# Optimization experiments

Measured on AMD Instinct MI355X. Metric: run time of the kernel, lower is better.

Reference implementation:

```python
import jax, jax.numpy as jnp
import numpy as np

B, T, D, H, L = 64, 4096, 128, 128, 2


def setup_inputs() -> dict:
    key = jax.random.key(0)
    ks = jax.random.split(key, 9)
    s = 1.0 / np.sqrt(H)
    return {
        "x": jax.random.normal(ks[0], (B, T, D), dtype=jnp.float32),
        "W_ih0": jax.random.normal(ks[1], (3 * H, D), dtype=jnp.float32) * s,
        "W_hh0": jax.random.normal(ks[2], (3 * H, H), dtype=jnp.float32) * s,
        "b_ih0": jax.random.normal(ks[3], (3 * H,), dtype=jnp.float32) * s,
        "b_hh0": jax.random.normal(ks[4], (3 * H,), dtype=jnp.float32) * s,
        "W_ih1": jax.random.normal(ks[5], (3 * H, H), dtype=jnp.float32) * s,
        "W_hh1": jax.random.normal(ks[6], (3 * H, H), dtype=jnp.float32) * s,
        "b_ih1": jax.random.normal(ks[7], (3 * H,), dtype=jnp.float32) * s,
        "b_hh1": jax.random.normal(ks[8], (3 * H,), dtype=jnp.float32) * s,
    }


def _gru_cell(h, xt, W_ih, W_hh, b_ih, b_hh):
    # torch.nn.GRUCell math; gates packed as [r, z, n] along 3H.
    gi = xt @ W_ih.T + b_ih            # [B, 3H]
    gh = h @ W_hh.T + b_hh             # [B, 3H]
    i_r, i_z, i_n = jnp.split(gi, 3, axis=-1)
    h_r, h_z, h_n = jnp.split(gh, 3, axis=-1)
    r = jax.nn.sigmoid(i_r + h_r)
    z = jax.nn.sigmoid(i_z + h_z)
    n = jnp.tanh(i_n + r * h_n)
    return (1.0 - z) * n + z * h


def reference(x, W_ih0, W_hh0, b_ih0, b_hh0, W_ih1, W_hh1, b_ih1, b_hh1):
    h0 = jnp.zeros((L, x.shape[0], H), dtype=x.dtype)
    params = ((W_ih0, W_hh0, b_ih0, b_hh0), (W_ih1, W_hh1, b_ih1, b_hh1))

    def step(h, xt):
        # h: [L, B, H]; xt: [B, D]
        inp = xt
        new_h = []
        for l in range(L):
            hl = _gru_cell(h[l], inp, *params[l])
            new_h.append(hl)
            inp = hl
        return jnp.stack(new_h, axis=0), None

    xs = jnp.swapaxes(x, 0, 1)  # [T, B, D]
    h_final, _ = jax.lax.scan(step, h0, xs)
    return h_final  # [L, B, H]
```

## Files before the change

### kernel.cpp

```cpp
#include <hip/hip_runtime.h>


#define Tlen 4096
#define Hd   128
#define Bsz  64

typedef __attribute__((ext_vector_type(8))) short short8;
typedef __attribute__((ext_vector_type(4))) short short4v;
typedef __attribute__((ext_vector_type(4))) float float4v;
typedef __attribute__((ext_vector_type(2))) unsigned int uint2v;

#define MFMA16(a, b, c) __builtin_amdgcn_mfma_f32_16x16x32_bf16((a), (b), (c), 0, 0, 0)

static __device__ __forceinline__ float fast_exp2(float x) {
#if __has_builtin(__builtin_amdgcn_exp2f)
  return __builtin_amdgcn_exp2f(x);
#else
  return exp2f(x);
#endif
}
static __device__ __forceinline__ float fast_rcp(float x) {
  return __builtin_amdgcn_rcpf(x);
}
static __device__ __forceinline__ short f2bf(float f) {
  unsigned u = __builtin_bit_cast(unsigned, f);
  u = (u + 0x7FFFu + ((u >> 16) & 1u)) >> 16;
  return (short)u;
}
static __device__ __forceinline__ unsigned pk2bf(float a, float b) {
#if __has_builtin(__builtin_amdgcn_cvt_pk_bf16_f32)
  auto v = __builtin_amdgcn_cvt_pk_bf16_f32(a, b);
  return __builtin_bit_cast(unsigned, v);
#else
  return (unsigned)(unsigned short)f2bf(a) | ((unsigned)(unsigned short)f2bf(b) << 16);
#endif
}
static __device__ __forceinline__ short8 loadw8(const float* __restrict__ p) {
  short8 r;
  #pragma unroll
  for (int j = 0; j < 8; ++j) r[j] = f2bf(p[j]);
  return r;
}

#define XB   0
#define H0B  4096
#define H1B  8192
#define BLK  2048

__global__ __launch_bounds__(512, 2) void gru_scan(
    const float* __restrict__ x,
    const float* __restrict__ Wih0, const float* __restrict__ Whh0,
    const float* __restrict__ bih0, const float* __restrict__ bhh0,
    const float* __restrict__ Wih1, const float* __restrict__ Whh1,
    const float* __restrict__ bih1, const float* __restrict__ bhh1,
    float* __restrict__ out) {
  __shared__ alignas(16) short Abuf[12288];

  const int tid   = threadIdx.x;
  const int wave  = tid >> 6;
  const int lane  = tid & 63;
  const int lc    = lane & 15;
  const int quad  = lane >> 4;
  const int q8    = quad * 8;
  const int lane8 = lane * 8;
  const int bbase = blockIdx.x * 16;

  const int wgrp = wave >> 2;
  const int w4   = wave & 3;

  const float* Wi = wgrp ? Wih1 : Wih0;
  const float* Wh = wgrp ? Whh1 : Whh0;
  const float* bi = wgrp ? bih1 : bih0;
  const float* bh = wgrp ? bhh1 : bhh0;

  short8 fxr[2][4], fxz[2][4], fxn[2][4];
  short8 fhr[2][4], fhz[2][4], fhn[2][4];
  float kr[2], kz[2], ki[2], kh[2];
  const float nL  = -1.44269504088896f;
  const float n2L = -2.88539008177793f;
  #pragma unroll
  for (int G = 0; G < 2; ++G) {
    const int c = 32 * w4 + 16 * G + lc;
    #pragma unroll
    for (int s = 0; s < 4; ++s) {
      const int k = 32 * s + q8;
      fxr[G][s] = loadw8(Wi + (c)       * Hd + k);
      fxz[G][s] = loadw8(Wi + (128 + c) * Hd + k);
      fxn[G][s] = loadw8(Wi + (256 + c) * Hd + k);
      fhr[G][s] = loadw8(Wh + (c)       * Hd + k);
      fhz[G][s] = loadw8(Wh + (128 + c) * Hd + k);
      fhn[G][s] = loadw8(Wh + (256 + c) * Hd + k);
    }
    kr[G] = nL  * (bi[c] + bh[c]);
    kz[G] = nL  * (bi[128 + c] + bh[128 + c]);
    ki[G] = n2L * bi[256 + c];
    kh[G] = n2L * bh[256 + c];
  }

  const int hsel = wgrp ? H1B : H0B;
  const int isel = wgrp ? H0B : XB;

  int hw[2];
  #pragma unroll
  for (int G = 0; G < 2; ++G)
    hw[G] = w4 * 512 + (2 * G + (lc >> 3)) * 128 + (lc & 7);

  const int xrow = tid >> 5;
  const int xk0  = 4 * (tid & 31);
  const int xwoff = (xk0 >> 5) * 512 + ((xk0 >> 3) & 3) * 128 + xrow * 8 + (xk0 & 7);
  const float* xg = x + (size_t)(bbase + xrow) * (Tlen * Hd) + xk0;

  const int glo = wgrp ? 2 : 0;
  const int ghi = glo + Tlen;

  {
    int* zb = (int*)Abuf;
    #pragma unroll
    for (int i = 0; i < 8; ++i) zb[2048 + tid + 512 * i] = 0;
    const float4v v0 = *(const float4v*)(xg);
    const float4v v1 = *(const float4v*)(xg + Hd);
    uint2v p0 = {pk2bf(v0[0], v0[1]), pk2bf(v0[2], v0[3])};
    uint2v p1 = {pk2bf(v1[0], v1[1]), pk2bf(v1[2], v1[3])};
    *(short4v*)&Abuf[XB + xwoff]       = __builtin_bit_cast(short4v, p0);
    *(short4v*)&Abuf[XB + BLK + xwoff] = __builtin_bit_cast(short4v, p1);
  }
  __syncthreads();

  const float4v Z4 = {0.f, 0.f, 0.f, 0.f};
  float4v ar[2], az[2], an[2], ah[2];
  float4v hp[2] = {Z4, Z4};

  #pragma unroll
  for (int G = 0; G < 2; ++G) { ar[G] = Z4; az[G] = Z4; an[G] = Z4; ah[G] = Z4; }
  #pragma unroll
  for (int s = 0; s < 4; ++s) {
    const short8 a = *(const short8*)&Abuf[isel + s * 512 + lane8];
    #pragma unroll
    for (int G = 0; G < 2; ++G) {
      ar[G] = MFMA16(a, fxr[G][s], ar[G]);
      az[G] = MFMA16(a, fxz[G][s], az[G]);
      an[G] = MFMA16(a, fxn[G][s], an[G]);
    }
  }

  for (int t = 0; t < Tlen + 2; ++t) {
    const int par  = (t & 1) * BLK;
    const int parx = BLK - par;

    const int tn = (t + 2 < Tlen) ? (t + 2) : (Tlen - 1);
    const float4v xv = *(const float4v*)(xg + (size_t)tn * Hd);
    const int hrd = hsel + parx;
    #pragma unroll
    for (int s = 0; s < 4; ++s) {
      const short8 a = *(const short8*)&Abuf[hrd + s * 512 + lane8];
      #pragma unroll
      for (int G = 0; G < 2; ++G) {
        ar[G] = MFMA16(a, fhr[G][s], ar[G]);
        az[G] = MFMA16(a, fhz[G][s], az[G]);
        ah[G] = MFMA16(a, fhn[G][s], ah[G]);
      }
    }
    __syncthreads();

    if (t >= glo && t < ghi) {
      const int wr = hsel + par;
      #pragma unroll
      for (int G = 0; G < 2; ++G) {
        #pragma unroll
        for (int i = 0; i < 4; ++i) {
          const float er = fast_exp2(fmaf(ar[G][i], nL, kr[G]));
          const float rr = fast_rcp(1.0f + er);
          const float ez = fast_exp2(fmaf(az[G][i], nL, kz[G]));
          const float zz = fast_rcp(1.0f + ez);
          float vv = fmaf(rr, fmaf(ah[G][i], n2L, kh[G]),
                          fmaf(an[G][i], n2L, ki[G]));
          vv = fminf(vv, 126.0f);
          const float e2 = fast_exp2(vv);
          const float nn = (1.0f - e2) * fast_rcp(1.0f + e2);
          const float hn = fmaf(zz, hp[G][i] - nn, nn);
          hp[G][i] = hn;
          Abuf[wr + hw[G] + (quad * 4 + i) * 8] = f2bf(hn);
        }
      }
    }
    {
      uint2v pp = {pk2bf(xv[0], xv[1]), pk2bf(xv[2], xv[3])};
      *(short4v*)&Abuf[XB + par + xwoff] = __builtin_bit_cast(short4v, pp);
    }
    const int ird = isel + parx;
    #pragma unroll
    for (int G = 0; G < 2; ++G) { ar[G] = Z4; az[G] = Z4; an[G] = Z4; ah[G] = Z4; }
    #pragma unroll
    for (int s = 0; s < 4; ++s) {
      const short8 a = *(const short8*)&Abuf[ird + s * 512 + lane8];
      #pragma unroll
      for (int G = 0; G < 2; ++G) {
        ar[G] = MFMA16(a, fxr[G][s], ar[G]);
        az[G] = MFMA16(a, fxz[G][s], az[G]);
        an[G] = MFMA16(a, fxn[G][s], an[G]);
      }
    }
    __syncthreads();
  }

  #pragma unroll
  for (int G = 0; G < 2; ++G) {
    const int u = 32 * w4 + 16 * G + lc;
    #pragma unroll
    for (int i = 0; i < 4; ++i) {
      const int b = bbase + quad * 4 + i;
      out[wgrp * (Bsz * Hd) + b * Hd + u] = hp[G][i];
    }
  }
}

extern "C" void kernel_launch(void* const* d_in, const int* in_sizes, int n_in,
                              void* d_out, int out_size, void* d_ws, size_t ws_size,
                              hipStream_t stream) {
  (void)in_sizes; (void)n_in; (void)out_size; (void)d_ws; (void)ws_size;
  gru_scan<<<4, 512, 0, stream>>>(
      (const float*)d_in[0],
      (const float*)d_in[1], (const float*)d_in[2],
      (const float*)d_in[3], (const float*)d_in[4],
      (const float*)d_in[5], (const float*)d_in[6],
      (const float*)d_in[7], (const float*)d_in[8],
      (float*)d_out);
}
```

Measured before the change: 7.165 ms.

## Double-buffer gate accumulators and interleave gate math with next-step input MFMAs

Splits the gate accumulators into two ping-pong sets and unrolls the time loop by two, so the next step's input-projection MFMAs can go into fresh registers while the current step's gate nonlinearities are still being computed. The gate math is interleaved between the per-slice input MFMAs so the transcendental/VALU work can overlap with matrix-core work. Accumulator zeroing is folded into the first MFMA. This raises register pressure (an extra set of six float4 accumulators) under a 512-thread, 2-blocks launch bound, which risks spills.

```diff
diff --git a/kernel.cpp b/kernel.cpp
--- a/kernel.cpp
+++ b/kernel.cpp
@@ -46,6 +46,73 @@
 #define H0B  4096
 #define H1B  8192
 #define BLK  2048
+
+#define GATE(CR, CZ, CN, G_, i_, wr_)                                       \
+  {                                                                         \
+    const float er = fast_exp2(fmaf(CR[G_][i_], nL, kr[G_]));               \
+    const float rr = fast_rcp(1.0f + er);                                   \
+    const float ez = fast_exp2(fmaf(CZ[G_][i_], nL, kz[G_]));               \
+    const float zz = fast_rcp(1.0f + ez);                                   \
+    float vv = fmaf(rr, fmaf(ahv[G_][i_], n2L, kh[G_]),                     \
+                    fmaf(CN[G_][i_], n2L, ki[G_]));                         \
+    vv = fminf(vv, 126.0f);                                                 \
+    const float e2 = fast_exp2(vv);                                         \
+    const float nn = (1.0f - e2) * fast_rcp(1.0f + e2);                     \
+    const float hn = fmaf(zz, hp[G_][i_] - nn, nn);                         \
+    hp[G_][i_] = hn;                                                        \
+    Abuf[(wr_) + hw[G_] + (quad * 4 + i_) * 8] = f2bf(hn);                  \
+  }
+
+#define STEP(t_, CR, CZ, CN, NR, NZ, NN)                                    \
+  {                                                                         \
+    const int par  = ((t_) & 1) * BLK;                                      \
+    const int parx = BLK - par;                                             \
+    const int tn = ((t_) + 2 < Tlen) ? ((t_) + 2) : (Tlen - 1);             \
+    const float4v xv = *(const float4v*)(xg + (size_t)tn * Hd);             \
+    const int hrd = hsel + parx;                                            \
+    _Pragma("unroll")                                                       \
+    for (int s = 0; s < 4; ++s) {                                           \
+      const short8 a = *(const short8*)&Abuf[hrd + s * 512 + lane8];        \
+      _Pragma("unroll")                                                     \
+      for (int G = 0; G < 2; ++G) {                                         \
+        CR[G] = MFMA16(a, fhr[G][s], CR[G]);                                \
+        CZ[G] = MFMA16(a, fhz[G][s], CZ[G]);                                \
+        ahv[G] = (s == 0) ? MFMA16(a, fhn[G][0], Z4)                        \
+                          : MFMA16(a, fhn[G][s], ahv[G]);                   \
+      }                                                                     \
+    }                                                                       \
+    __syncthreads();                                                        \
+    {                                                                       \
+      uint2v pp = {pk2bf(xv[0], xv[1]), pk2bf(xv[2], xv[3])};               \
+      *(short4v*)&Abuf[XB + par + xwoff] = __builtin_bit_cast(short4v, pp); \
+    }                                                                       \
+    const bool gv = ((t_) >= glo) & ((t_) < ghi);                           \
+    const int wr  = hsel + par;                                             \
+    const int ird = isel + parx;                                            \
+    _Pragma("unroll")                                                       \
+    for (int s = 0; s < 4; ++s) {                                           \
+      const short8 a = *(const short8*)&Abuf[ird + s * 512 + lane8];        \
+      if (gv) {                                                             \
+        _Pragma("unroll")                                                   \
+        for (int ii = 0; ii < 2; ++ii) {                                    \
+          GATE(CR, CZ, CN, (s >> 1), ((s & 1) * 2 + ii), wr);               \
+        }                                                                   \
+      }                                                                     \
+      _Pragma("unroll")                                                     \
+      for (int G = 0; G < 2; ++G) {                                         \
+        if (s == 0) {                                                       \
+          NR[G] = MFMA16(a, fxr[G][0], Z4);                                 \
+          NZ[G] = MFMA16(a, fxz[G][0], Z4);                                 \
+          NN[G] = MFMA16(a, fxn[G][0], Z4);                                 \
+        } else {                                                            \
+          NR[G] = MFMA16(a, fxr[G][s], NR[G]);                              \
+          NZ[G] = MFMA16(a, fxz[G][s], NZ[G]);                              \
+          NN[G] = MFMA16(a, fxn[G][s], NN[G]);                              \
+        }                                                                   \
+      }                                                                     \
+    }                                                                       \
+    __syncthreads();                                                        \
+  }
 
 __global__ __launch_bounds__(512, 2) void gru_scan(
     const float* __restrict__ x,
@@ -127,80 +194,30 @@
   __syncthreads();
 
   const float4v Z4 = {0.f, 0.f, 0.f, 0.f};
-  float4v ar[2], az[2], an[2], ah[2];
-  float4v hp[2] = {Z4, Z4};
-
-  #pragma unroll
-  for (int G = 0; G < 2; ++G) { ar[G] = Z4; az[G] = Z4; an[G] = Z4; ah[G] = Z4; }
+  float4v arA[2], azA[2], anA[2];
+  float4v arB[2], azB[2], anB[2];
+  float4v ahv[2], hp[2] = {Z4, Z4};
+
   #pragma unroll
   for (int s = 0; s < 4; ++s) {
     const short8 a = *(const short8*)&Abuf[isel + s * 512 + lane8];
     #pragma unroll
     for (int G = 0; G < 2; ++G) {
-      ar[G] = MFMA16(a, fxr[G][s], ar[G]);
-      az[G] = MFMA16(a, fxz[G][s], az[G]);
-      an[G] = MFMA16(a, fxn[G][s], an[G]);
-    }
-  }
-
-  for (int t = 0; t < Tlen + 2; ++t) {
-    const int par  = (t & 1) * BLK;
-    const int parx = BLK - par;
-
-    const int tn = (t + 2 < Tlen) ? (t + 2) : (Tlen - 1);
-    const float4v xv = *(const float4v*)(xg + (size_t)tn * Hd);
-    const int hrd = hsel + parx;
-    #pragma unroll
-    for (int s = 0; s < 4; ++s) {
-      const short8 a = *(const short8*)&Abuf[hrd + s * 512 + lane8];
-      #pragma unroll
-      for (int G = 0; G < 2; ++G) {
-        ar[G] = MFMA16(a, fhr[G][s], ar[G]);
-        az[G] = MFMA16(a, fhz[G][s], az[G]);
-        ah[G] = MFMA16(a, fhn[G][s], ah[G]);
+      if (s == 0) {
+        arA[G] = MFMA16(a, fxr[G][0], Z4);
+        azA[G] = MFMA16(a, fxz[G][0], Z4);
+        anA[G] = MFMA16(a, fxn[G][0], Z4);
+      } else {
+        arA[G] = MFMA16(a, fxr[G][s], arA[G]);
+        azA[G] = MFMA16(a, fxz[G][s], azA[G]);
+        anA[G] = MFMA16(a, fxn[G][s], anA[G]);
       }
     }
-    __syncthreads();
-
-    if (t >= glo && t < ghi) {
-      const int wr = hsel + par;
-      #pragma unroll
-      for (int G = 0; G < 2; ++G) {
-        #pragma unroll
-        for (int i = 0; i < 4; ++i) {
-          const float er = fast_exp2(fmaf(ar[G][i], nL, kr[G]));
-          const float rr = fast_rcp(1.0f + er);
-          const float ez = fast_exp2(fmaf(az[G][i], nL, kz[G]));
-          const float zz = fast_rcp(1.0f + ez);
-          float vv = fmaf(rr, fmaf(ah[G][i], n2L, kh[G]),
-                          fmaf(an[G][i], n2L, ki[G]));
-          vv = fminf(vv, 126.0f);
-          const float e2 = fast_exp2(vv);
-          const float nn = (1.0f - e2) * fast_rcp(1.0f + e2);
-          const float hn = fmaf(zz, hp[G][i] - nn, nn);
-          hp[G][i] = hn;
-          Abuf[wr + hw[G] + (quad * 4 + i) * 8] = f2bf(hn);
-        }
-      }
-    }
-    {
-      uint2v pp = {pk2bf(xv[0], xv[1]), pk2bf(xv[2], xv[3])};
-      *(short4v*)&Abuf[XB + par + xwoff] = __builtin_bit_cast(short4v, pp);
-    }
-    const int ird = isel + parx;
-    #pragma unroll
-    for (int G = 0; G < 2; ++G) { ar[G] = Z4; az[G] = Z4; an[G] = Z4; ah[G] = Z4; }
-    #pragma unroll
-    for (int s = 0; s < 4; ++s) {
-      const short8 a = *(const short8*)&Abuf[ird + s * 512 + lane8];
-      #pragma unroll
-      for (int G = 0; G < 2; ++G) {
-        ar[G] = MFMA16(a, fxr[G][s], ar[G]);
-        az[G] = MFMA16(a, fxz[G][s], az[G]);
-        an[G] = MFMA16(a, fxn[G][s], an[G]);
-      }
-    }
-    __syncthreads();
+  }
+
+  for (int tt = 0; tt < Tlen + 2; tt += 2) {
+    STEP(tt,     arA, azA, anA, arB, azB, anB);
+    STEP(tt + 1, arB, azB, anB, arA, azA, anA);
   }
 
   #pragma unroll
```

After: 13.37 ms. 1.87x slower.

## Stagger layer-0 and layer-1 wave groups across barrier phases to overlap work

Applied to the files above, without the earlier changes.

Reorganizes the per-timestep schedule so the two wave groups (layer 0 and layer 1) do their gate math and MFMAs in opposite halves between the two barriers. Layer 1's elementwise update now runs while layer 0 does its recurrent MFMAs, and the reverse, with layer 1 lagging by an extra step. The aim is to stop both groups from hitting the serial elementwise phase at once, keeping the MFMA and VALU pipes busy together. It also moves x staging to layer-0 waves only, using 8-wide loads and packed bf16 stores. The cost is one extra loop iteration and more complex buffer-parity bookkeeping.

```diff
diff --git a/kernel.cpp b/kernel.cpp
--- a/kernel.cpp
+++ b/kernel.cpp
@@ -8,7 +8,7 @@
 typedef __attribute__((ext_vector_type(8))) short short8;
 typedef __attribute__((ext_vector_type(4))) short short4v;
 typedef __attribute__((ext_vector_type(4))) float float4v;
-typedef __attribute__((ext_vector_type(2))) unsigned int uint2v;
+typedef __attribute__((ext_vector_type(4))) unsigned int uint4v;
 
 #define MFMA16(a, b, c) __builtin_amdgcn_mfma_f32_16x16x32_bf16((a), (b), (c), 0, 0, 0)
 
@@ -34,6 +34,11 @@
 #else
   return (unsigned)(unsigned short)f2bf(a) | ((unsigned)(unsigned short)f2bf(b) << 16);
 #endif
+}
+static __device__ __forceinline__ short8 pk8(float4v a, float4v b) {
+  uint4v u = {pk2bf(a[0], a[1]), pk2bf(a[2], a[3]),
+              pk2bf(b[0], b[1]), pk2bf(b[2], b[3])};
+  return __builtin_bit_cast(short8, u);
 }
 static __device__ __forceinline__ short8 loadw8(const float* __restrict__ p) {
   short8 r;
@@ -105,99 +110,150 @@
   for (int G = 0; G < 2; ++G)
     hw[G] = w4 * 512 + (2 * G + (lc >> 3)) * 128 + (lc & 7);
 
-  const int xrow = tid >> 5;
-  const int xk0  = 4 * (tid & 31);
-  const int xwoff = (xk0 >> 5) * 512 + ((xk0 >> 3) & 3) * 128 + xrow * 8 + (xk0 & 7);
-  const float* xg = x + (size_t)(bbase + xrow) * (Tlen * Hd) + xk0;
-
-  const int glo = wgrp ? 2 : 0;
-  const int ghi = glo + Tlen;
+  const int xrow  = tid >> 4;
+  const int xk0   = (tid & 15) * 8;
+  const int xwoff = (xk0 >> 5) * 512 + ((xk0 >> 3) & 3) * 128 + xrow * 8;
+  const float* xg = x + (size_t)(bbase + (xrow & 15)) * (Tlen * Hd) + xk0;
 
   {
     int* zb = (int*)Abuf;
     #pragma unroll
     for (int i = 0; i < 8; ++i) zb[2048 + tid + 512 * i] = 0;
-    const float4v v0 = *(const float4v*)(xg);
-    const float4v v1 = *(const float4v*)(xg + Hd);
-    uint2v p0 = {pk2bf(v0[0], v0[1]), pk2bf(v0[2], v0[3])};
-    uint2v p1 = {pk2bf(v1[0], v1[1]), pk2bf(v1[2], v1[3])};
-    *(short4v*)&Abuf[XB + xwoff]       = __builtin_bit_cast(short4v, p0);
-    *(short4v*)&Abuf[XB + BLK + xwoff] = __builtin_bit_cast(short4v, p1);
+    if (wgrp == 0) {
+      const float4v a0 = *(const float4v*)(xg);
+      const float4v b0 = *(const float4v*)(xg + 4);
+      const float4v a1 = *(const float4v*)(xg + Hd);
+      const float4v b1 = *(const float4v*)(xg + Hd + 4);
+      *(short8*)&Abuf[XB + xwoff]       = pk8(a0, b0);
+      *(short8*)&Abuf[XB + BLK + xwoff] = pk8(a1, b1);
+    }
   }
   __syncthreads();
 
   const float4v Z4 = {0.f, 0.f, 0.f, 0.f};
   float4v ar[2], az[2], an[2], ah[2];
   float4v hp[2] = {Z4, Z4};
-
   #pragma unroll
   for (int G = 0; G < 2; ++G) { ar[G] = Z4; az[G] = Z4; an[G] = Z4; ah[G] = Z4; }
-  #pragma unroll
-  for (int s = 0; s < 4; ++s) {
-    const short8 a = *(const short8*)&Abuf[isel + s * 512 + lane8];
-    #pragma unroll
-    for (int G = 0; G < 2; ++G) {
-      ar[G] = MFMA16(a, fxr[G][s], ar[G]);
-      az[G] = MFMA16(a, fxz[G][s], az[G]);
-      an[G] = MFMA16(a, fxn[G][s], an[G]);
-    }
-  }
-
-  for (int t = 0; t < Tlen + 2; ++t) {
-    const int par  = (t & 1) * BLK;
-    const int parx = BLK - par;
-
-    const int tn = (t + 2 < Tlen) ? (t + 2) : (Tlen - 1);
-    const float4v xv = *(const float4v*)(xg + (size_t)tn * Hd);
-    const int hrd = hsel + parx;
+
+  if (wgrp == 0) {
     #pragma unroll
     for (int s = 0; s < 4; ++s) {
-      const short8 a = *(const short8*)&Abuf[hrd + s * 512 + lane8];
-      #pragma unroll
-      for (int G = 0; G < 2; ++G) {
-        ar[G] = MFMA16(a, fhr[G][s], ar[G]);
-        az[G] = MFMA16(a, fhz[G][s], az[G]);
-        ah[G] = MFMA16(a, fhn[G][s], ah[G]);
-      }
-    }
-    __syncthreads();
-
-    if (t >= glo && t < ghi) {
-      const int wr = hsel + par;
-      #pragma unroll
-      for (int G = 0; G < 2; ++G) {
-        #pragma unroll
-        for (int i = 0; i < 4; ++i) {
-          const float er = fast_exp2(fmaf(ar[G][i], nL, kr[G]));
-          const float rr = fast_rcp(1.0f + er);
-          const float ez = fast_exp2(fmaf(az[G][i], nL, kz[G]));
-          const float zz = fast_rcp(1.0f + ez);
-          float vv = fmaf(rr, fmaf(ah[G][i], n2L, kh[G]),
-                          fmaf(an[G][i], n2L, ki[G]));
-          vv = fminf(vv, 126.0f);
-          const float e2 = fast_exp2(vv);
-          const float nn = (1.0f - e2) * fast_rcp(1.0f + e2);
-          const float hn = fmaf(zz, hp[G][i] - nn, nn);
-          hp[G][i] = hn;
-          Abuf[wr + hw[G] + (quad * 4 + i) * 8] = f2bf(hn);
-        }
-      }
-    }
-    {
-      uint2v pp = {pk2bf(xv[0], xv[1]), pk2bf(xv[2], xv[3])};
-      *(short4v*)&Abuf[XB + par + xwoff] = __builtin_bit_cast(short4v, pp);
-    }
-    const int ird = isel + parx;
-    #pragma unroll
-    for (int G = 0; G < 2; ++G) { ar[G] = Z4; az[G] = Z4; an[G] = Z4; ah[G] = Z4; }
-    #pragma unroll
-    for (int s = 0; s < 4; ++s) {
-      const short8 a = *(const short8*)&Abuf[ird + s * 512 + lane8];
+      const short8 a = *(const short8*)&Abuf[XB + s * 512 + lane8];
       #pragma unroll
       for (int G = 0; G < 2; ++G) {
         ar[G] = MFMA16(a, fxr[G][s], ar[G]);
         az[G] = MFMA16(a, fxz[G][s], az[G]);
         an[G] = MFMA16(a, fxn[G][s], an[G]);
+      }
+    }
+  }
+
+  for (int t = 0; t < Tlen + 3; ++t) {
+    const int par  = (t & 1) * BLK;
+    const int parx = BLK - par;
+    float4v xv0, xv1;
+
+    if (wgrp == 0) {
+      const int tn = (t + 2 < Tlen) ? (t + 2) : (Tlen - 1);
+      xv0 = *(const float4v*)(xg + (size_t)tn * Hd);
+      xv1 = *(const float4v*)(xg + (size_t)tn * Hd + 4);
+      const int hrd = hsel + parx;
+      #pragma unroll
+      for (int s = 0; s < 4; ++s) {
+        const short8 a = *(const short8*)&Abuf[hrd + s * 512 + lane8];
+        #pragma unroll
+        for (int G = 0; G < 2; ++G) {
+          ar[G] = MFMA16(a, fhr[G][s], ar[G]);
+          az[G] = MFMA16(a, fhz[G][s], az[G]);
+          ah[G] = MFMA16(a, fhn[G][s], ah[G]);
+        }
+      }
+    } else {
+      if (t >= 3) {
+        const int wr = hsel + parx;
+        #pragma unroll
+        for (int G = 0; G < 2; ++G) {
+          #pragma unroll
+          for (int i = 0; i < 4; ++i) {
+            const float er = fast_exp2(fmaf(ar[G][i], nL, kr[G]));
+            const float rr = fast_rcp(1.0f + er);
+            const float ez = fast_exp2(fmaf(az[G][i], nL, kz[G]));
+            const float zz = fast_rcp(1.0f + ez);
+            float vv = fmaf(rr, fmaf(ah[G][i], n2L, kh[G]),
+                            fmaf(an[G][i], n2L, ki[G]));
+            vv = fminf(vv, 126.0f);
+            const float e2 = fast_exp2(vv);
+            const float nn = (1.0f - e2) * fast_rcp(1.0f + e2);
+            const float hn = fmaf(zz, hp[G][i] - nn, nn);
+            hp[G][i] = hn;
+            Abuf[wr + hw[G] + (quad * 4 + i) * 8] = f2bf(hn);
+          }
+        }
+      }
+      const int ird = isel + par;
+      #pragma unroll
+      for (int G = 0; G < 2; ++G) { ar[G] = Z4; az[G] = Z4; an[G] = Z4; ah[G] = Z4; }
+      #pragma unroll
+      for (int s = 0; s < 4; ++s) {
+        const short8 a = *(const short8*)&Abuf[ird + s * 512 + lane8];
+        #pragma unroll
+        for (int G = 0; G < 2; ++G) {
+          ar[G] = MFMA16(a, fxr[G][s], ar[G]);
+          az[G] = MFMA16(a, fxz[G][s], az[G]);
+          an[G] = MFMA16(a, fxn[G][s], an[G]);
+        }
+      }
+    }
+    __syncthreads();
+
+    if (wgrp == 0) {
+      *(short8*)&Abuf[XB + par + xwoff] = pk8(xv0, xv1);
+      if (t < Tlen) {
+        const int wr = hsel + par;
+        #pragma unroll
+        for (int G = 0; G < 2; ++G) {
+          #pragma unroll
+          for (int i = 0; i < 4; ++i) {
+            const float er = fast_exp2(fmaf(ar[G][i], nL, kr[G]));
+            const float rr = fast_rcp(1.0f + er);
+            const float ez = fast_exp2(fmaf(az[G][i], nL, kz[G]));
+            const float zz = fast_rcp(1.0f + ez);
+            float vv = fmaf(rr, fmaf(ah[G][i], n2L, kh[G]),
+                            fmaf(an[G][i], n2L, ki[G]));
+            vv = fminf(vv, 126.0f);
+            const float e2 = fast_exp2(vv);
+            const float nn = (1.0f - e2) * fast_rcp(1.0f + e2);
+            const float hn = fmaf(zz, hp[G][i] - nn, nn);
+            hp[G][i] = hn;
+            Abuf[wr + hw[G] + (quad * 4 + i) * 8] = f2bf(hn);
+          }
+        }
+      }
+      const int ird = isel + parx;
+      #pragma unroll
+      for (int G = 0; G < 2; ++G) { ar[G] = Z4; az[G] = Z4; an[G] = Z4; ah[G] = Z4; }
+      #pragma unroll
+      for (int s = 0; s < 4; ++s) {
+        const short8 a = *(const short8*)&Abuf[ird + s * 512 + lane8];
+        #pragma unroll
+        for (int G = 0; G < 2; ++G) {
+          ar[G] = MFMA16(a, fxr[G][s], ar[G]);
+          az[G] = MFMA16(a, fxz[G][s], az[G]);
+          an[G] = MFMA16(a, fxn[G][s], an[G]);
+        }
+      }
+    } else {
+      const int hrd = hsel + parx;
+      #pragma unroll
+      for (int s = 0; s < 4; ++s) {
+        const short8 a = *(const short8*)&Abuf[hrd + s * 512 + lane8];
+        #pragma unroll
+        for (int G = 0; G < 2; ++G) {
+          ar[G] = MFMA16(a, fhr[G][s], ar[G]);
+          az[G] = MFMA16(a, fhz[G][s], az[G]);
+          ah[G] = MFMA16(a, fhn[G][s], ah[G]);
+        }
       }
     }
     __syncthreads();
```

Result: slower. 14.94 ms (+108.6%).
